# Kernel tuning notes

Measured on AMD Instinct MI355X. Metric: run time of the kernel, lower is better.

The kernel has to match this reference:

```python
import jax, jax.numpy as jnp
import numpy as np

B, L, D = 4, 2048, 512   # batch, seq_len, model_dim
H, A = 8, 64             # head_num, atten_dim (H*A == D)
EPS = 1e-5


def setup_inputs() -> dict:
    key = jax.random.key(0)
    ks = jax.random.split(key, 20)
    std = 1.0 / np.sqrt(D)
    inp = {}
    for i, name in enumerate(["Q_data", "Q_time", "K_data", "K_time", "V_time"]):
        inp[name] = jax.random.normal(ks[i], (B, L, D), dtype=jnp.float32)
    # projection params (torch Linear: y = x @ W.T + b); store as [in, out]
    for i, name in enumerate(["Wq_d", "Wq_t", "Wk_d", "Wk_t", "Wv_t", "Wo"]):
        inp[name + "_w"] = jax.random.uniform(ks[5 + i], (D, H * A), jnp.float32, -std, std)
        inp[name + "_b"] = jax.random.uniform(ks[11 + i], (H * A,), jnp.float32, -std, std)
    inp["ln_g"] = jnp.ones((D,), jnp.float32)
    inp["ln_b"] = jnp.zeros((D,), jnp.float32)
    return inp


def _proj(x, w, b):
    # [B,L,D] -> [B,H,L,A]
    y = jnp.einsum('bld,de->ble', x, w) + b
    return y.reshape(B, L, H, A).transpose(0, 2, 1, 3)


def reference(Q_data, Q_time, K_data, K_time, V_time,
              Wq_d_w, Wq_t_w, Wk_d_w, Wk_t_w, Wv_t_w, Wo_w,
              Wq_d_b, Wq_t_b, Wk_d_b, Wk_t_b, Wv_t_b, Wo_b,
              ln_g, ln_b):
    residual = Q_data
    qd = _proj(Q_data, Wq_d_w, Wq_d_b)
    qt = _proj(Q_time, Wq_t_w, Wq_t_b)
    kd = _proj(K_data, Wk_d_w, Wk_d_b)
    kt = _proj(K_time, Wk_t_w, Wk_t_b)
    vt = _proj(V_time, Wv_t_w, Wv_t_b)
    scale = 1.0 / np.sqrt(A)
    # dual QK^T scores summed before softmax
    scores = (jnp.einsum('bhqa,bhka->bhqk', qd, kd)
              + jnp.einsum('bhqa,bhka->bhqk', qt, kt)) * scale
    attn = jax.nn.softmax(scores, axis=-1)
    ctx = jnp.einsum('bhqk,bhka->bhqa', attn, vt)        # [B,H,L,A]
    ctx = ctx.transpose(0, 2, 1, 3).reshape(B, L, H * A)  # [B,L,D]
    out = jnp.einsum('bld,de->ble', ctx, Wo_w) + Wo_b
    x = out + residual
    mu = jnp.mean(x, axis=-1, keepdims=True)
    var = jnp.var(x, axis=-1, keepdims=True)
    return (x - mu) / jnp.sqrt(var + EPS) * ln_g + ln_b
```

## Files before the change

### kernel.cpp

```cpp
#include <hip/hip_runtime.h>
#include <hip/hip_bf16.h>
#include <stdint.h>


using f32x4  = __attribute__((ext_vector_type(4))) float;
using bf16x8 = __attribute__((ext_vector_type(8))) short;

typedef __attribute__((address_space(1))) const uint32_t g_u32;
typedef __attribute__((address_space(3))) uint32_t l_u32;

#if __has_builtin(__builtin_amdgcn_exp2f)
#define EXP2F __builtin_amdgcn_exp2f
#else
#define EXP2F exp2f
#endif
#define QSCALE 0.1803368801111204f

__device__ __forceinline__ void glds16(const void* g, void* l) {
  __builtin_amdgcn_global_load_lds((g_u32*)g, (l_u32*)l, 16, 0, 0);
}

__device__ __forceinline__ unsigned short f2bfu(float f) {
  __hip_bfloat16 h = __float2bfloat16(f);
  union { __hip_bfloat16 h; unsigned short u; } v;
  v.h = h;
  return v.u;
}

__device__ __forceinline__ uint32_t pack_trunc(float lo, float hi) {
  union { float f; uint32_t u; } a, b;
  a.f = lo; b.f = hi;
  return __builtin_amdgcn_perm(b.u, a.u, 0x07060302u);
}

__global__ __launch_bounds__(256) void k_prep_w(
    const float* __restrict__ w0, const float* __restrict__ w1,
    const float* __restrict__ w2, const float* __restrict__ w3,
    const float* __restrict__ w4, const float* __restrict__ w5,
    unsigned short* __restrict__ wt) {
  __shared__ float tile[64][68];
  const float* wsrc[6] = {w0, w1, w2, w3, w4, w5};
  int bid = blockIdx.x;
  int mat = bid >> 6, tid = bid & 63;
  int k0 = (tid >> 3) << 6, c0 = (tid & 7) << 6;
  const float* w = wsrc[mat];
  int t = threadIdx.x;
  {
    int r = t >> 2, cq = (t & 3) << 4;
    const float4* src = reinterpret_cast<const float4*>(w + (size_t)(k0 + r) * 512 + c0 + cq);
#pragma unroll
    for (int j = 0; j < 4; ++j) {
      float4 v = src[j];
      tile[r][cq + j * 4 + 0] = v.x;
      tile[r][cq + j * 4 + 1] = v.y;
      tile[r][cq + j * 4 + 2] = v.z;
      tile[r][cq + j * 4 + 3] = v.w;
    }
  }
  __syncthreads();
  {
    int cc = t >> 2, kq = (t & 3) << 4;
    union { unsigned short u[16]; uint4 v[2]; } p;
#pragma unroll
    for (int j = 0; j < 16; ++j) p.u[j] = f2bfu(tile[kq + j][cc]);
    unsigned short* dst = wt + (size_t)mat * 262144 + (size_t)(c0 + cc) * 512 + k0 + kq;
    *reinterpret_cast<uint4*>(dst)     = p.v[0];
    *reinterpret_cast<uint4*>(dst + 8) = p.v[1];
  }
}

__global__ __launch_bounds__(512) void k_proj2(
    const float* __restrict__ x0, const float* __restrict__ x1,
    const float* __restrict__ x2, const float* __restrict__ x3,
    const float* __restrict__ x4,
    const unsigned short* __restrict__ wt,
    const float* __restrict__ b0, const float* __restrict__ b1,
    const float* __restrict__ b2, const float* __restrict__ b3,
    const float* __restrict__ b4,
    unsigned short* __restrict__ qws, unsigned short* __restrict__ kws,
    unsigned short* __restrict__ vws) {
  __shared__ __align__(16) unsigned short Abuf[8192];
  __shared__ __align__(16) unsigned short Bbuf[2][8192];
  int bid = blockIdx.x;
  int proj = bid >> 8, rem = bid & 255;
  int cb = rem >> 6, rb = rem & 63;
  const float* xs[5] = {x0, x1, x2, x3, x4};
  const float* Ag = xs[proj] + (size_t)rb * 128 * 512;
  const unsigned short* Wg = wt + (size_t)proj * 262144 + (size_t)cb * 128 * 512;
  int t = threadIdx.x;
  int lane = t & 63, w = t >> 6, wr = w >> 2, wc = w & 3, g = lane >> 4, c = lane & 15;
  f32x4 acc[4][2];
#pragma unroll
  for (int i = 0; i < 4; ++i)
#pragma unroll
    for (int j = 0; j < 2; ++j) acc[i][j] = f32x4{0.f, 0.f, 0.f, 0.f};

  int srow[2], sch[2];
#pragma unroll
  for (int j = 0; j < 2; ++j) {
    int q = t + j * 512;
    srow[j] = q >> 3;
    sch[j] = q & 7;
  }
  float4 pa[2], pb[2];
#pragma unroll
  for (int j = 0; j < 2; ++j) {
    const float* src = Ag + (size_t)srow[j] * 512 + sch[j] * 8;
    pa[j] = *reinterpret_cast<const float4*>(src);
    pb[j] = *reinterpret_cast<const float4*>(src + 4);
  }
#pragma unroll
  for (int j = 0; j < 2; ++j) {
    int cid = t + j * 512;
    int row = cid >> 3, ch = cid & 7;
    glds16(Wg + (size_t)row * 512 + ((ch ^ (row & 7)) << 3), &Bbuf[0][cid * 8]);
  }

#pragma unroll 1
  for (int it = 0; it < 8; ++it) {
    int cur = it & 1;
    __syncthreads();
#pragma unroll
    for (int j = 0; j < 2; ++j) {
      union { unsigned short u[8]; uint4 v; } p;
      p.u[0] = f2bfu(pa[j].x); p.u[1] = f2bfu(pa[j].y);
      p.u[2] = f2bfu(pa[j].z); p.u[3] = f2bfu(pa[j].w);
      p.u[4] = f2bfu(pb[j].x); p.u[5] = f2bfu(pb[j].y);
      p.u[6] = f2bfu(pb[j].z); p.u[7] = f2bfu(pb[j].w);
      *reinterpret_cast<uint4*>(&Abuf[srow[j] * 64 + ((sch[j] ^ (srow[j] & 7)) << 3)]) = p.v;
    }
    __syncthreads();
    if (it < 7) {
#pragma unroll
      for (int j = 0; j < 2; ++j) {
        const float* src = Ag + (size_t)srow[j] * 512 + (it + 1) * 64 + sch[j] * 8;
        pa[j] = *reinterpret_cast<const float4*>(src);
        pb[j] = *reinterpret_cast<const float4*>(src + 4);
      }
#pragma unroll
      for (int j = 0; j < 2; ++j) {
        int cid = t + j * 512;
        int row = cid >> 3, ch = cid & 7;
        glds16(Wg + (size_t)row * 512 + (it + 1) * 64 + ((ch ^ (row & 7)) << 3),
               &Bbuf[cur ^ 1][cid * 8]);
      }
    }
#pragma unroll
    for (int fi = 0; fi < 2; ++fi) {
      bf16x8 af[4], bfr[2];
#pragma unroll
      for (int mi = 0; mi < 4; ++mi) {
        int arow = wr * 64 + mi * 16 + c;
        af[mi] = *reinterpret_cast<const bf16x8*>(
            &Abuf[arow * 64 + (((fi * 4 + g) ^ (arow & 7)) << 3)]);
      }
#pragma unroll
      for (int ni = 0; ni < 2; ++ni) {
        int brow = wc * 32 + ni * 16 + c;
        bfr[ni] = *reinterpret_cast<const bf16x8*>(
            &Bbuf[cur][brow * 64 + (((fi * 4 + g) ^ (brow & 7)) << 3)]);
      }
      __builtin_amdgcn_s_setprio(1);
#pragma unroll
      for (int mi = 0; mi < 4; ++mi)
#pragma unroll
        for (int ni = 0; ni < 2; ++ni)
          acc[mi][ni] = __builtin_amdgcn_mfma_f32_16x16x32_bf16(af[mi], bfr[ni], acc[mi][ni], 0, 0, 0);
      __builtin_amdgcn_s_setprio(0);
    }
  }

  const float* bias_arr[5] = {b0, b1, b2, b3, b4};
  const float* bias = bias_arr[proj];
  float scale = (proj < 2) ? QSCALE : 1.0f;
  unsigned short* qkdst = (proj < 2) ? qws : kws;
  int half = (proj & 1) ? 64 : 0;
#pragma unroll
  for (int ni = 0; ni < 2; ++ni) {
    int n = wc * 32 + ni * 16 + c;
    int h = cb * 2 + (n >> 6);
    int a = n & 63;
    float bv = bias[cb * 128 + n];
#pragma unroll
    for (int mi = 0; mi < 4; ++mi) {
#pragma unroll
      for (int rr = 0; rr < 4; ++rr) {
        float v = (acc[mi][ni][rr] + bv) * scale;
        unsigned short u = f2bfu(v);
        int rowg = rb * 128 + wr * 64 + mi * 16 + g * 4 + rr;
        int b = rowg >> 11, l = rowg & 2047;
        if (proj < 4) {
          qkdst[((size_t)(b * 8 + h) * 2048 + l) * 128 + half + a] = u;
        } else {
          vws[((size_t)(b * 8 + h) * 64 + a) * 2048 + l] = u;
        }
      }
    }
  }
}

__device__ __forceinline__ void gemm_core(
    const unsigned short* Ag, const unsigned short* Wg,
    unsigned short* Al, unsigned short* Bl, f32x4 acc[4]) {
  int t = threadIdx.x;
  int lane = t & 63, w = t >> 6, g = lane >> 4, c = lane & 15;
#pragma unroll 1
  for (int it = 0; it < 8; ++it) {
    __syncthreads();
#pragma unroll
    for (int j = 0; j < 2; ++j) {
      int cid = t + j * 256;
      int row = cid >> 3, ch = cid & 7;
      glds16(Ag + (size_t)row * 512 + it * 64 + ((ch ^ (row & 7)) << 3), Al + cid * 8);
      glds16(Wg + (size_t)row * 512 + it * 64 + ((ch ^ (row & 7)) << 3), Bl + cid * 8);
    }
    __syncthreads();
#pragma unroll
    for (int fi = 0; fi < 2; ++fi) {
      int arow = w * 16 + c;
      bf16x8 af = *reinterpret_cast<const bf16x8*>(
          Al + arow * 64 + (((fi * 4 + g) ^ (arow & 7)) << 3));
#pragma unroll
      for (int ct = 0; ct < 4; ++ct) {
        int brow = ct * 16 + c;
        bf16x8 bf = *reinterpret_cast<const bf16x8*>(
            Bl + brow * 64 + (((fi * 4 + g) ^ (brow & 7)) << 3));
        acc[ct] = __builtin_amdgcn_mfma_f32_16x16x32_bf16(af, bf, acc[ct], 0, 0, 0);
      }
    }
  }
}

__global__ __launch_bounds__(256) void k_attn(
    const unsigned short* __restrict__ qws, const unsigned short* __restrict__ kws,
    const unsigned short* __restrict__ vws, unsigned short* __restrict__ ctxb) {
  __shared__ __align__(16) unsigned short Kb[2][8192];
  __shared__ __align__(16) unsigned short Vb[2][4096];
  int orig = blockIdx.x;
  int xcd = orig & 7, j = orig >> 3;
  int bh = xcd * 4 + (j >> 4), qb = j & 15;
  int t = threadIdx.x;
  int w = t >> 6, lane = t & 63, g = lane >> 4, c = lane & 15;

  const unsigned short* Kg = kws + (size_t)bh * 2048 * 128;
  const unsigned short* Vg = vws + (size_t)bh * 64 * 2048;

  bf16x8 qf[2][4];
#pragma unroll
  for (int qt = 0; qt < 2; ++qt) {
    const unsigned short* Qg =
        qws + ((size_t)bh * 2048 + qb * 128 + w * 32 + qt * 16 + c) * 128;
#pragma unroll
    for (int fi = 0; fi < 4; ++fi)
      qf[qt][fi] = *reinterpret_cast<const bf16x8*>(Qg + fi * 32 + g * 8);
  }

  f32x4 o[2][4];
#pragma unroll
  for (int qt = 0; qt < 2; ++qt)
#pragma unroll
    for (int at = 0; at < 4; ++at) o[qt][at] = f32x4{0.f, 0.f, 0.f, 0.f};
  float lsum[2] = {0.f, 0.f};

#pragma unroll
  for (int jj = 0; jj < 4; ++jj) {
    int cid = t + jj * 256;
    int row = cid >> 4, ch = cid & 15;
    glds16(Kg + (size_t)row * 128 + ((ch ^ (row & 15)) << 3), &Kb[0][cid * 8]);
  }
#pragma unroll
  for (int jj = 0; jj < 2; ++jj) {
    int cid = t + jj * 256;
    int a = cid >> 3, ch = cid & 7;
    glds16(Vg + (size_t)a * 2048 + ((ch ^ (a & 7)) << 3), &Vb[0][cid * 8]);
  }
  __syncthreads();

#pragma unroll 1
  for (int it = 0; it < 32; ++it) {
    int cur = it & 1;
    if (it < 31) {
      int nxt = cur ^ 1;
#pragma unroll
      for (int jj = 0; jj < 4; ++jj) {
        int cid = t + jj * 256;
        int row = cid >> 4, ch = cid & 15;
        glds16(Kg + ((size_t)(it + 1) * 64 + row) * 128 + ((ch ^ (row & 15)) << 3),
               &Kb[nxt][cid * 8]);
      }
#pragma unroll
      for (int jj = 0; jj < 2; ++jj) {
        int cid = t + jj * 256;
        int a = cid >> 3, ch = cid & 7;
        glds16(Vg + (size_t)a * 2048 + (it + 1) * 64 + ((ch ^ (a & 7)) << 3),
               &Vb[nxt][cid * 8]);
      }
    }

    f32x4 s[2][4];
#pragma unroll
    for (int qt = 0; qt < 2; ++qt)
#pragma unroll
      for (int mt = 0; mt < 4; ++mt) s[qt][mt] = f32x4{0.f, 0.f, 0.f, 0.f};
#pragma unroll
    for (int fi = 0; fi < 4; ++fi) {
      bf16x8 kf[4];
#pragma unroll
      for (int mt = 0; mt < 4; ++mt)
        kf[mt] = *reinterpret_cast<const bf16x8*>(
            &Kb[cur][(mt * 16 + c) * 128 + (((fi * 4 + g) ^ c) << 3)]);
      __builtin_amdgcn_s_setprio(1);
#pragma unroll
      for (int mt = 0; mt < 4; ++mt) {
        s[0][mt] = __builtin_amdgcn_mfma_f32_16x16x32_bf16(kf[mt], qf[0][fi], s[0][mt], 0, 0, 0);
        s[1][mt] = __builtin_amdgcn_mfma_f32_16x16x32_bf16(kf[mt], qf[1][fi], s[1][mt], 0, 0, 0);
      }
      __builtin_amdgcn_s_setprio(0);
    }

    uint32_t pku[2][4][2];
#pragma unroll
    for (int qt = 0; qt < 2; ++qt) {
      float ls = 0.f;
#pragma unroll
      for (int mt = 0; mt < 4; ++mt) {
        float p0 = EXP2F(s[qt][mt][0]);
        float p1 = EXP2F(s[qt][mt][1]);
        float p2 = EXP2F(s[qt][mt][2]);
        float p3 = EXP2F(s[qt][mt][3]);
        ls += (p0 + p1) + (p2 + p3);
        pku[qt][mt][0] = pack_trunc(p0, p1);
        pku[qt][mt][1] = pack_trunc(p2, p3);
      }
      lsum[qt] += ls;
    }

    union u32x4_bf { uint32_t u[4]; bf16x8 v; };
    u32x4_bf pf[2][2];
#pragma unroll
    for (int qt = 0; qt < 2; ++qt) {
      pf[qt][0].u[0] = pku[qt][0][0]; pf[qt][0].u[1] = pku[qt][0][1];
      pf[qt][0].u[2] = pku[qt][1][0]; pf[qt][0].u[3] = pku[qt][1][1];
      pf[qt][1].u[0] = pku[qt][2][0]; pf[qt][1].u[1] = pku[qt][2][1];
      pf[qt][1].u[2] = pku[qt][3][0]; pf[qt][1].u[3] = pku[qt][3][1];
    }
#pragma unroll
    for (int at = 0; at < 4; ++at) {
      int arow = at * 16 + c;
      u32x4_bf vf0, vf1;
#pragma unroll
      for (int pp = 0; pp < 2; ++pp) {
        int ch0 = (2 * pp + (g >> 1)) ^ (arow & 7);
        int ch1 = (4 + 2 * pp + (g >> 1)) ^ (arow & 7);
        uint2 d0 = *reinterpret_cast<const uint2*>(
            &Vb[cur][arow * 64 + ch0 * 8 + ((g & 1) << 2)]);
        uint2 d1 = *reinterpret_cast<const uint2*>(
            &Vb[cur][arow * 64 + ch1 * 8 + ((g & 1) << 2)]);
        vf0.u[2 * pp] = d0.x; vf0.u[2 * pp + 1] = d0.y;
        vf1.u[2 * pp] = d1.x; vf1.u[2 * pp + 1] = d1.y;
      }
      __builtin_amdgcn_s_setprio(1);
#pragma unroll
      for (int qt = 0; qt < 2; ++qt) {
        o[qt][at] = __builtin_amdgcn_mfma_f32_16x16x32_bf16(pf[qt][0].v, vf0.v, o[qt][at], 0, 0, 0);
        o[qt][at] = __builtin_amdgcn_mfma_f32_16x16x32_bf16(pf[qt][1].v, vf1.v, o[qt][at], 0, 0, 0);
      }
      __builtin_amdgcn_s_setprio(0);
    }
    __syncthreads();
  }

  int b = bh >> 3, h = bh & 7;
#pragma unroll
  for (int qt = 0; qt < 2; ++qt) {
    lsum[qt] += __shfl_xor(lsum[qt], 16);
    lsum[qt] += __shfl_xor(lsum[qt], 32);
    float rinv[4];
#pragma unroll
    for (int r = 0; r < 4; ++r) rinv[r] = 1.0f / __shfl(lsum[qt], g * 4 + r);
    int rowg0 = b * 2048 + qb * 128 + w * 32 + qt * 16 + g * 4;
#pragma unroll
    for (int at = 0; at < 4; ++at)
#pragma unroll
      for (int r = 0; r < 4; ++r) {
        float v = o[qt][at][r] * rinv[r];
        ctxb[(size_t)(rowg0 + r) * 512 + h * 64 + at * 16 + c] = f2bfu(v);
      }
  }
}

__global__ __launch_bounds__(256) void k_oproj(
    const unsigned short* __restrict__ ctxb, const unsigned short* __restrict__ wt,
    const float* __restrict__ bo, const float* __restrict__ resid,
    float* __restrict__ out) {
  __shared__ __align__(16) unsigned short Al[4096];
  __shared__ __align__(16) unsigned short Bl[4096];
  int bid = blockIdx.x;
  int rb = bid >> 3, cb = bid & 7;
  const unsigned short* Ag = ctxb + (size_t)rb * 64 * 512;
  const unsigned short* Wg = wt + (size_t)5 * 262144 + (size_t)cb * 64 * 512;
  f32x4 acc[4];
#pragma unroll
  for (int i = 0; i < 4; ++i) acc[i] = f32x4{0.f, 0.f, 0.f, 0.f};
  gemm_core(Ag, Wg, Al, Bl, acc);
  int lane = threadIdx.x & 63, w = threadIdx.x >> 6, g = lane >> 4, c = lane & 15;
  int rowbase = rb * 64 + w * 16 + g * 4;
#pragma unroll
  for (int ct = 0; ct < 4; ++ct) {
    int n = cb * 64 + ct * 16 + c;
    float bv = bo[n];
#pragma unroll
    for (int r = 0; r < 4; ++r) {
      int rowg = rowbase + r;
      size_t di = (size_t)rowg * 512 + n;
      out[di] = acc[ct][r] + bv + resid[di];
    }
  }
}

__global__ __launch_bounds__(256) void k_ln(float* __restrict__ out,
                                            const float* __restrict__ gam,
                                            const float* __restrict__ bet) {
  int row = blockIdx.x * 4 + (threadIdx.x >> 6);
  int lane = threadIdx.x & 63;
  float* x = out + (size_t)row * 512 + lane * 8;
  float4 v0 = reinterpret_cast<const float4*>(x)[0];
  float4 v1 = reinterpret_cast<const float4*>(x)[1];
  float s = v0.x + v0.y + v0.z + v0.w + v1.x + v1.y + v1.z + v1.w;
  float q = v0.x * v0.x + v0.y * v0.y + v0.z * v0.z + v0.w * v0.w +
            v1.x * v1.x + v1.y * v1.y + v1.z * v1.z + v1.w * v1.w;
#pragma unroll
  for (int d = 1; d < 64; d <<= 1) {
    s += __shfl_xor(s, d);
    q += __shfl_xor(q, d);
  }
  float mu = s * (1.0f / 512.0f);
  float var = q * (1.0f / 512.0f) - mu * mu;
  float rstd = rsqrtf(var + 1e-5f);
  float4 g0 = reinterpret_cast<const float4*>(gam + lane * 8)[0];
  float4 g1 = reinterpret_cast<const float4*>(gam + lane * 8)[1];
  float4 b0 = reinterpret_cast<const float4*>(bet + lane * 8)[0];
  float4 b1 = reinterpret_cast<const float4*>(bet + lane * 8)[1];
  v0.x = (v0.x - mu) * rstd * g0.x + b0.x;
  v0.y = (v0.y - mu) * rstd * g0.y + b0.y;
  v0.z = (v0.z - mu) * rstd * g0.z + b0.z;
  v0.w = (v0.w - mu) * rstd * g0.w + b0.w;
  v1.x = (v1.x - mu) * rstd * g1.x + b1.x;
  v1.y = (v1.y - mu) * rstd * g1.y + b1.y;
  v1.z = (v1.z - mu) * rstd * g1.z + b1.z;
  v1.w = (v1.w - mu) * rstd * g1.w + b1.w;
  reinterpret_cast<float4*>(x)[0] = v0;
  reinterpret_cast<float4*>(x)[1] = v1;
}

extern "C" void kernel_launch(void* const* d_in, const int* in_sizes, int n_in,
                              void* d_out, int out_size, void* d_ws, size_t ws_size,
                              hipStream_t stream) {
  const float* Qd  = (const float*)d_in[0];
  const float* Qt  = (const float*)d_in[1];
  const float* Kd  = (const float*)d_in[2];
  const float* Kt  = (const float*)d_in[3];
  const float* Vt  = (const float*)d_in[4];
  const float* Wqd = (const float*)d_in[5];
  const float* bqd = (const float*)d_in[6];
  const float* Wqt = (const float*)d_in[7];
  const float* bqt = (const float*)d_in[8];
  const float* Wkd = (const float*)d_in[9];
  const float* bkd = (const float*)d_in[10];
  const float* Wkt = (const float*)d_in[11];
  const float* bkt = (const float*)d_in[12];
  const float* Wvt = (const float*)d_in[13];
  const float* bvt = (const float*)d_in[14];
  const float* Wo  = (const float*)d_in[15];
  const float* bo  = (const float*)d_in[16];
  const float* lng = (const float*)d_in[17];
  const float* lnb = (const float*)d_in[18];

  char* ws = (char*)d_ws;
  unsigned short* wt   = (unsigned short*)(ws);
  unsigned short* qws  = (unsigned short*)(ws + 3145728);
  unsigned short* kws  = (unsigned short*)(ws + 19922944);
  unsigned short* vws  = (unsigned short*)(ws + 36700160);
  unsigned short* ctxb = (unsigned short*)(ws + 45088768);
  float* out = (float*)d_out;

  k_prep_w<<<384, 256, 0, stream>>>(Wqd, Wqt, Wkd, Wkt, Wvt, Wo, wt);
  k_proj2<<<1280, 512, 0, stream>>>(Qd, Qt, Kd, Kt, Vt, wt,
                                    bqd, bqt, bkd, bkt, bvt, qws, kws, vws);
  k_attn<<<512, 256, 0, stream>>>(qws, kws, vws, ctxb);
  k_oproj<<<1024, 256, 0, stream>>>(ctxb, wt, bo, Qd, out);
  k_ln<<<2048, 256, 0, stream>>>(out, lng, lnb);
}
```

Measured before the change: 133.2 us.

## Stream fp32 activations to LDS asynchronously in projection GEMM, convert at fragment load

The projection kernel now loads the fp32 activation tile straight into LDS with async global-to-LDS copies, double-buffered like the weight tile. The bf16 conversion (truncating pack) moves to the fragment read, replacing the register prefetch, convert and LDS store step and one barrier per iteration. The tile changes from 128x128 with 512 threads to 64x128 with 256 threads, doubling the block count. This costs twice the LDS footprint for A, extra LDS read bandwidth for fp32 data and truncation instead of round-to-nearest for activations.

```diff
diff --git a/kernel.cpp b/kernel.cpp
--- a/kernel.cpp
+++ b/kernel.cpp
@@ -69,7 +69,7 @@
   }
 }
 
-__global__ __launch_bounds__(512) void k_proj2(
+__global__ __launch_bounds__(256) void k_proj2(
     const float* __restrict__ x0, const float* __restrict__ x1,
     const float* __restrict__ x2, const float* __restrict__ x3,
     const float* __restrict__ x4,
@@ -79,95 +79,88 @@
     const float* __restrict__ b4,
     unsigned short* __restrict__ qws, unsigned short* __restrict__ kws,
     unsigned short* __restrict__ vws) {
-  __shared__ __align__(16) unsigned short Abuf[8192];
-  __shared__ __align__(16) unsigned short Bbuf[2][8192];
+  __shared__ __align__(16) float Af[2][4096];
+  __shared__ __align__(16) unsigned short Bb[2][8192];
   int bid = blockIdx.x;
-  int proj = bid >> 8, rem = bid & 255;
-  int cb = rem >> 6, rb = rem & 63;
+  int proj = bid >> 9, rem = bid & 511;
+  int cb = rem >> 7, rb = rem & 127;
   const float* xs[5] = {x0, x1, x2, x3, x4};
-  const float* Ag = xs[proj] + (size_t)rb * 128 * 512;
+  const float* Ag = xs[proj] + (size_t)rb * 64 * 512;
   const unsigned short* Wg = wt + (size_t)proj * 262144 + (size_t)cb * 128 * 512;
   int t = threadIdx.x;
-  int lane = t & 63, w = t >> 6, wr = w >> 2, wc = w & 3, g = lane >> 4, c = lane & 15;
-  f32x4 acc[4][2];
-#pragma unroll
-  for (int i = 0; i < 4; ++i)
-#pragma unroll
-    for (int j = 0; j < 2; ++j) acc[i][j] = f32x4{0.f, 0.f, 0.f, 0.f};
-
-  int srow[2], sch[2];
-#pragma unroll
-  for (int j = 0; j < 2; ++j) {
-    int q = t + j * 512;
-    srow[j] = q >> 3;
-    sch[j] = q & 7;
-  }
-  float4 pa[2], pb[2];
-#pragma unroll
-  for (int j = 0; j < 2; ++j) {
-    const float* src = Ag + (size_t)srow[j] * 512 + sch[j] * 8;
-    pa[j] = *reinterpret_cast<const float4*>(src);
-    pb[j] = *reinterpret_cast<const float4*>(src + 4);
-  }
-#pragma unroll
-  for (int j = 0; j < 2; ++j) {
-    int cid = t + j * 512;
-    int row = cid >> 3, ch = cid & 7;
-    glds16(Wg + (size_t)row * 512 + ((ch ^ (row & 7)) << 3), &Bbuf[0][cid * 8]);
-  }
+  int lane = t & 63, w = t >> 6, g = lane >> 4, c = lane & 15;
+  int wm = w >> 1, wn = w & 1;
+  f32x4 acc[2][4];
+#pragma unroll
+  for (int i = 0; i < 2; ++i)
+#pragma unroll
+    for (int j = 0; j < 4; ++j) acc[i][j] = f32x4{0.f, 0.f, 0.f, 0.f};
+
+#pragma unroll
+  for (int j = 0; j < 4; ++j) {
+    int q = t + j * 256;
+    int row = q >> 4, ch = q & 15;
+    glds16(Ag + (size_t)row * 512 + ((ch ^ (row & 15)) << 2), &Af[0][q * 4]);
+  }
+#pragma unroll
+  for (int j = 0; j < 4; ++j) {
+    int q = t + j * 256;
+    int row = q >> 3, ch = q & 7;
+    glds16(Wg + (size_t)row * 512 + ((ch ^ (row & 7)) << 3), &Bb[0][q * 8]);
+  }
+  __syncthreads();
 
 #pragma unroll 1
   for (int it = 0; it < 8; ++it) {
     int cur = it & 1;
+    if (it < 7) {
+      int nxt = cur ^ 1;
+#pragma unroll
+      for (int j = 0; j < 4; ++j) {
+        int q = t + j * 256;
+        int row = q >> 4, ch = q & 15;
+        glds16(Ag + (size_t)row * 512 + (it + 1) * 64 + ((ch ^ (row & 15)) << 2),
+               &Af[nxt][q * 4]);
+      }
+#pragma unroll
+      for (int j = 0; j < 4; ++j) {
+        int q = t + j * 256;
+        int row = q >> 3, ch = q & 7;
+        glds16(Wg + (size_t)row * 512 + (it + 1) * 64 + ((ch ^ (row & 7)) << 3),
+               &Bb[nxt][q * 8]);
+      }
+    }
+#pragma unroll
+    for (int fi = 0; fi < 2; ++fi) {
+      union uab { uint32_t u[4]; bf16x8 v; } af[2];
+#pragma unroll
+      for (int mi = 0; mi < 2; ++mi) {
+        int arow = wm * 32 + mi * 16 + c;
+        int r = arow & 15;
+        int c0 = (fi * 4 + g) * 2;
+        f32x4 q0 = *reinterpret_cast<const f32x4*>(&Af[cur][arow * 64 + ((c0 ^ r) << 2)]);
+        f32x4 q1 = *reinterpret_cast<const f32x4*>(&Af[cur][arow * 64 + (((c0 + 1) ^ r) << 2)]);
+        af[mi].u[0] = pack_trunc(q0[0], q0[1]);
+        af[mi].u[1] = pack_trunc(q0[2], q0[3]);
+        af[mi].u[2] = pack_trunc(q1[0], q1[1]);
+        af[mi].u[3] = pack_trunc(q1[2], q1[3]);
+      }
+      bf16x8 bfr[4];
+#pragma unroll
+      for (int ni = 0; ni < 4; ++ni) {
+        int brow = wn * 64 + ni * 16 + c;
+        bfr[ni] = *reinterpret_cast<const bf16x8*>(
+            &Bb[cur][brow * 64 + (((fi * 4 + g) ^ (brow & 7)) << 3)]);
+      }
+      __builtin_amdgcn_s_setprio(1);
+#pragma unroll
+      for (int mi = 0; mi < 2; ++mi)
+#pragma unroll
+        for (int ni = 0; ni < 4; ++ni)
+          acc[mi][ni] = __builtin_amdgcn_mfma_f32_16x16x32_bf16(af[mi].v, bfr[ni], acc[mi][ni], 0, 0, 0);
+      __builtin_amdgcn_s_setprio(0);
+    }
     __syncthreads();
-#pragma unroll
-    for (int j = 0; j < 2; ++j) {
-      union { unsigned short u[8]; uint4 v; } p;
-      p.u[0] = f2bfu(pa[j].x); p.u[1] = f2bfu(pa[j].y);
-      p.u[2] = f2bfu(pa[j].z); p.u[3] = f2bfu(pa[j].w);
-      p.u[4] = f2bfu(pb[j].x); p.u[5] = f2bfu(pb[j].y);
-      p.u[6] = f2bfu(pb[j].z); p.u[7] = f2bfu(pb[j].w);
-      *reinterpret_cast<uint4*>(&Abuf[srow[j] * 64 + ((sch[j] ^ (srow[j] & 7)) << 3)]) = p.v;
-    }
-    __syncthreads();
-    if (it < 7) {
-#pragma unroll
-      for (int j = 0; j < 2; ++j) {
-        const float* src = Ag + (size_t)srow[j] * 512 + (it + 1) * 64 + sch[j] * 8;
-        pa[j] = *reinterpret_cast<const float4*>(src);
-        pb[j] = *reinterpret_cast<const float4*>(src + 4);
-      }
-#pragma unroll
-      for (int j = 0; j < 2; ++j) {
-        int cid = t + j * 512;
-        int row = cid >> 3, ch = cid & 7;
-        glds16(Wg + (size_t)row * 512 + (it + 1) * 64 + ((ch ^ (row & 7)) << 3),
-               &Bbuf[cur ^ 1][cid * 8]);
-      }
-    }
-#pragma unroll
-    for (int fi = 0; fi < 2; ++fi) {
-      bf16x8 af[4], bfr[2];
-#pragma unroll
-      for (int mi = 0; mi < 4; ++mi) {
-        int arow = wr * 64 + mi * 16 + c;
-        af[mi] = *reinterpret_cast<const bf16x8*>(
-            &Abuf[arow * 64 + (((fi * 4 + g) ^ (arow & 7)) << 3)]);
-      }
-#pragma unroll
-      for (int ni = 0; ni < 2; ++ni) {
-        int brow = wc * 32 + ni * 16 + c;
-        bfr[ni] = *reinterpret_cast<const bf16x8*>(
-            &Bbuf[cur][brow * 64 + (((fi * 4 + g) ^ (brow & 7)) << 3)]);
-      }
-      __builtin_amdgcn_s_setprio(1);
-#pragma unroll
-      for (int mi = 0; mi < 4; ++mi)
-#pragma unroll
-        for (int ni = 0; ni < 2; ++ni)
-          acc[mi][ni] = __builtin_amdgcn_mfma_f32_16x16x32_bf16(af[mi], bfr[ni], acc[mi][ni], 0, 0, 0);
-      __builtin_amdgcn_s_setprio(0);
-    }
   }
 
   const float* bias_arr[5] = {b0, b1, b2, b3, b4};
@@ -175,19 +168,18 @@
   float scale = (proj < 2) ? QSCALE : 1.0f;
   unsigned short* qkdst = (proj < 2) ? qws : kws;
   int half = (proj & 1) ? 64 : 0;
-#pragma unroll
-  for (int ni = 0; ni < 2; ++ni) {
-    int n = wc * 32 + ni * 16 + c;
-    int h = cb * 2 + (n >> 6);
-    int a = n & 63;
-    float bv = bias[cb * 128 + n];
-#pragma unroll
-    for (int mi = 0; mi < 4; ++mi) {
+  int h = cb * 2 + wn;
+#pragma unroll
+  for (int ni = 0; ni < 4; ++ni) {
+    int a = ni * 16 + c;
+    float bv = bias[h * 64 + a];
+#pragma unroll
+    for (int mi = 0; mi < 2; ++mi) {
 #pragma unroll
       for (int rr = 0; rr < 4; ++rr) {
         float v = (acc[mi][ni][rr] + bv) * scale;
         unsigned short u = f2bfu(v);
-        int rowg = rb * 128 + wr * 64 + mi * 16 + g * 4 + rr;
+        int rowg = rb * 64 + wm * 32 + mi * 16 + g * 4 + rr;
         int b = rowg >> 11, l = rowg & 2047;
         if (proj < 4) {
           qkdst[((size_t)(b * 8 + h) * 2048 + l) * 128 + half + a] = u;
@@ -485,7 +477,7 @@
   float* out = (float*)d_out;
 
   k_prep_w<<<384, 256, 0, stream>>>(Wqd, Wqt, Wkd, Wkt, Wvt, Wo, wt);
-  k_proj2<<<1280, 512, 0, stream>>>(Qd, Qt, Kd, Kt, Vt, wt,
+  k_proj2<<<2560, 256, 0, stream>>>(Qd, Qt, Kd, Kt, Vt, wt,
                                     bqd, bqt, bkd, bkt, bvt, qws, kws, vws);
   k_attn<<<512, 256, 0, stream>>>(qws, kws, vws, ctxb);
   k_oproj<<<1024, 256, 0, stream>>>(ctxb, wt, bo, Qd, out);
```

New measurement: 145.4 us. +9.1%, slower.
